# Optimization experiments

Hardware: AMD Instinct MI355X
Metric: run time of the kernel (lower is better)

Reference implementation:

```python
import jax, jax.numpy as jnp
import numpy as np

CODEBOOK_SIZE = 8192
EMBED_DIM = 128
BETA = 0.25


def setup_inputs() -> dict:
    key = jax.random.key(0)
    k1, k2 = jax.random.split(key)
    z = jax.random.normal(k1, (8, 4096, EMBED_DIM), dtype=jnp.float32)
    # nn.Embedding weight init: uniform(-1/embedding_dim, 1/embedding_dim)
    emb = jax.random.uniform(
        k2, (CODEBOOK_SIZE, EMBED_DIM), dtype=jnp.float32,
        minval=-1.0 / EMBED_DIM, maxval=1.0 / EMBED_DIM)
    return {"z": z, "emb": emb}


def reference(z, emb):
    sg = jax.lax.stop_gradient
    zf = z.reshape(-1, EMBED_DIM)                      # [N, D]
    # squared-distance: |z|^2 + |e|^2 - 2 z.e^T  -> [N, K]
    d = (jnp.sum(zf * zf, axis=1, keepdims=True)
         + jnp.sum(emb * emb, axis=1)
         - 2.0 * jnp.einsum('nd,kd->nk', zf, emb))
    idx = jnp.argmin(d, axis=1)                        # [N]
    z_q = emb[idx].reshape(z.shape)                    # gather + reshape

    # codebook usage perplexity (bincount)
    counts = jnp.zeros(CODEBOOK_SIZE, dtype=jnp.float32).at[idx].add(1.0)
    e_mean = counts / idx.size
    perplexity = jnp.exp(-jnp.sum(e_mean * jnp.log(e_mean + 1e-8)))

    commit_loss = (BETA * jnp.mean((sg(z_q) - z) ** 2)
                   + jnp.mean((z_q - sg(z)) ** 2))
    z_q_st = z + sg(z_q - z)                           # straight-through
    return z_q_st, commit_loss, perplexity
```

## Files before the change

### kernel.cpp

```cpp
#include <hip/hip_runtime.h>
#include <float.h>
#include <math.h>

#define DIM    128
#define KCB    8192
#define BT     128
#define NC     128
#define NCHUNK (KCB / NC)

typedef __attribute__((ext_vector_type(8))) short bf16x8;
typedef __attribute__((ext_vector_type(4))) float f32x4;

__device__ unsigned g_ehi[KCB * DIM / 2];
__device__ unsigned g_elo[KCB * DIM / 2];
__device__ float    g_h[KCB];
__device__ unsigned g_counts[KCB];
__device__ double   g_loss;

__device__ __forceinline__ unsigned short f2b(float x) {
    union { float f; unsigned u; } v; v.f = x;
    unsigned r = v.u + 0x7fffu + ((v.u >> 16) & 1u);
    return (unsigned short)(r >> 16);
}
__device__ __forceinline__ float b2f(unsigned short h) {
    union { unsigned u; float f; } v; v.u = ((unsigned)h) << 16; return v.f;
}
__device__ __forceinline__ void gll16(const void* g, void* l) {
    __builtin_amdgcn_global_load_lds(
        (const __attribute__((address_space(1))) void*)g,
        (__attribute__((address_space(3))) void*)l, 16, 0, 0);
}

__global__ __launch_bounds__(256) void vq_prep(const float* __restrict__ emb)
{
    const int tid  = threadIdx.x;
    const int gid  = blockIdx.x * 256 + tid;
    if (gid < KCB) g_counts[gid] = 0u;
    if (gid == 0)  g_loss = 0.0;

    const int code = (blockIdx.x << 2) + (tid >> 6);
    const int lane = tid & 63;
    const float2 v = ((const float2*)emb)[code * 64 + lane];

    unsigned short h0 = f2b(v.x), h1 = f2b(v.y);
    unsigned short l0 = f2b(v.x - b2f(h0)), l1 = f2b(v.y - b2f(h1));
    const int widx = code * 64 + (lane ^ ((code & 7) << 2));
    g_ehi[widx] = (unsigned)h0 | ((unsigned)h1 << 16);
    g_elo[widx] = (unsigned)l0 | ((unsigned)l1 << 16);

    float s = v.x * v.x + v.y * v.y;
    #pragma unroll
    for (int o = 32; o > 0; o >>= 1) s += __shfl_down(s, o);
    if (lane == 0) g_h[code] = 0.5f * s;
}

__global__ __launch_bounds__(512, 1) void vq_main(
    const float* __restrict__ z, const float* __restrict__ emb, float* __restrict__ out)
{
    __shared__ char   smem[2 * 65536];
    __shared__ float  rv[BT * 2];
    __shared__ int    ri[BT * 2];
    __shared__ int    idx_sh[BT];
    __shared__ double wred[8];

    const int tid  = threadIdx.x;
    const int lane = tid & 63;
    const int wid  = tid >> 6;
    const int tq   = wid & 3;
    const int ch2  = wid >> 2;
    const int l15  = lane & 15;
    const int lg   = lane >> 4;
    const long t0  = (long)blockIdx.x * BT;

    bf16x8 ah[2][4], al[2][4];
    #pragma unroll
    for (int m = 0; m < 2; ++m) {
        const long trow = t0 + tq * 32 + m * 16 + l15;
        #pragma unroll
        for (int kk = 0; kk < 4; ++kk) {
            const float4* zp = (const float4*)(z + trow * DIM + kk * 32 + lg * 8);
            float4 v0 = zp[0], v1 = zp[1];
            float xs[8] = {v0.x, v0.y, v0.z, v0.w, v1.x, v1.y, v1.z, v1.w};
            #pragma unroll
            for (int j = 0; j < 8; ++j) {
                unsigned short hb = f2b(xs[j]);
                ah[m][kk][j] = (short)hb;
                al[m][kk][j] = (short)f2b(xs[j] - b2f(hb));
            }
        }
    }

    const int xr = (l15 & 7) << 4;
    int loff[4];
    #pragma unroll
    for (int kk = 0; kk < 4; ++kk) loff[kk] = l15 * 256 + ((kk * 64 + lg * 16) ^ xr);
    const int nwave = ch2 * 64 * 256;

    float bv[2][4]; int bi[2][4];
    #pragma unroll
    for (int m = 0; m < 2; ++m)
        #pragma unroll
        for (int r = 0; r < 4; ++r) { bv[m][r] = FLT_MAX; bi[m][r] = 0; }

    {
        const int o = tid * 16;
        #pragma unroll
        for (int r = 0; r < 4; ++r)
            gll16((const char*)g_ehi + r * 8192 + o, smem + r * 8192 + o);
        #pragma unroll
        for (int r = 0; r < 4; ++r)
            gll16((const char*)g_elo + r * 8192 + o, smem + 32768 + r * 8192 + o);
    }
    __syncthreads();

    for (int ch = 0; ch < NCHUNK; ++ch) {
        const int cb  = ch * NC;
        const int cur = ch & 1;
        if (ch + 1 < NCHUNK) {
            const int   o  = tid * 16;
            const long  go = (long)(ch + 1) * 32768;
            char* ldst = smem + (cur ^ 1) * 65536;
            #pragma unroll
            for (int r = 0; r < 4; ++r)
                gll16((const char*)g_ehi + go + r * 8192 + o, ldst + r * 8192 + o);
            #pragma unroll
            for (int r = 0; r < 4; ++r)
                gll16((const char*)g_elo + go + r * 8192 + o, ldst + 32768 + r * 8192 + o);
        }

        const char* bhi = smem + cur * 65536 + nwave;
        const char* blo = bhi + 32768;

        #pragma unroll
        for (int n = 0; n < 4; ++n) {
            bf16x8 bh[4], bl[4];
            #pragma unroll
            for (int kk = 0; kk < 4; ++kk) {
                bh[kk] = *(const bf16x8*)(bhi + n * 4096 + loff[kk]);
                bl[kk] = *(const bf16x8*)(blo + n * 4096 + loff[kk]);
            }
            f32x4 acc[2];
            #pragma unroll
            for (int m = 0; m < 2; ++m) {
                f32x4 a = {0.f, 0.f, 0.f, 0.f};
                #pragma unroll
                for (int kk = 0; kk < 4; ++kk) {
                    a = __builtin_amdgcn_mfma_f32_16x16x32_bf16(ah[m][kk], bh[kk], a, 0, 0, 0);
                    a = __builtin_amdgcn_mfma_f32_16x16x32_bf16(al[m][kk], bh[kk], a, 0, 0, 0);
                    a = __builtin_amdgcn_mfma_f32_16x16x32_bf16(ah[m][kk], bl[kk], a, 0, 0, 0);
                }
                acc[m] = a;
            }
            const int c  = cb + ch2 * 64 + n * 16 + l15;
            const float hc = g_h[c];
            #pragma unroll
            for (int m = 0; m < 2; ++m)
                #pragma unroll
                for (int r = 0; r < 4; ++r) {
                    float sc = hc - acc[m][r];
                    if (sc < bv[m][r]) { bv[m][r] = sc; bi[m][r] = c; }
                }
        }
        __syncthreads();
    }

    #pragma unroll
    for (int m = 0; m < 2; ++m)
        #pragma unroll
        for (int r = 0; r < 4; ++r) {
            float v = bv[m][r]; int ix = bi[m][r];
            #pragma unroll
            for (int o = 1; o < 16; o <<= 1) {
                float ov = __shfl_xor(v, o);
                int   oi = __shfl_xor(ix, o);
                if (ov < v || (ov == v && oi < ix)) { v = ov; ix = oi; }
            }
            if (l15 == 0) {
                int t = tq * 32 + m * 16 + lg * 4 + r;
                rv[t * 2 + ch2] = v; ri[t * 2 + ch2] = ix;
            }
        }
    __syncthreads();
    if (tid < BT) {
        float v0 = rv[tid * 2], v1 = rv[tid * 2 + 1];
        int   i0 = ri[tid * 2], i1 = ri[tid * 2 + 1];
        int best = (v1 < v0 || (v1 == v0 && i1 < i0)) ? i1 : i0;
        idx_sh[tid] = best;
        atomicAdd(&g_counts[best], 1u);
    }
    __syncthreads();

    float lsum = 0.f;
    {
        const float4* zf4 = (const float4*)(z + t0 * DIM);
        const float4* ef4 = (const float4*)emb;
        float4*       of4 = (float4*)(out + t0 * DIM);
        #pragma unroll
        for (int r = 0; r < 8; ++r) {
            int f = r * 512 + tid;
            int t = f >> 5, dw = f & 31;
            int ci = idx_sh[t];
            float4 e4 = ef4[(size_t)ci * 32 + dw];
            float4 z4 = zf4[f];
            float dx = e4.x - z4.x, dy = e4.y - z4.y;
            float dz = e4.z - z4.z, dw2 = e4.w - z4.w;
            lsum += dx * dx + dy * dy + dz * dz + dw2 * dw2;
            float4 o;
            o.x = z4.x + dx; o.y = z4.y + dy; o.z = z4.z + dz; o.w = z4.w + dw2;
            of4[f] = o;
        }
    }
    #pragma unroll
    for (int o = 32; o > 0; o >>= 1) lsum += __shfl_down(lsum, o);
    if (lane == 0) wred[wid] = (double)lsum;
    __syncthreads();
    if (tid == 0) {
        double s = 0.0;
        #pragma unroll
        for (int w = 0; w < 8; ++w) s += wred[w];
        atomicAdd(&g_loss, s);
    }
}

__global__ __launch_bounds__(256) void vq_final(float* __restrict__ out, int n_elems, int n_tok)
{
    __shared__ double sh[4];
    const int tid = threadIdx.x;
    double s = 0.0;
    for (int i = tid; i < KCB; i += 256) {
        float em = (float)g_counts[i] / (float)n_tok;
        s += (double)(em * logf(em + 1e-8f));
    }
    #pragma unroll
    for (int o = 32; o > 0; o >>= 1) s += __shfl_down(s, o);
    if ((tid & 63) == 0) sh[tid >> 6] = s;
    __syncthreads();
    if (tid == 0) {
        double tot = sh[0] + sh[1] + sh[2] + sh[3];
        out[(size_t)n_elems]     = (float)(1.25 * g_loss / (double)n_elems);
        out[(size_t)n_elems + 1] = expf((float)(-tot));
    }
}

extern "C" void kernel_launch(void* const* d_in, const int* in_sizes, int n_in,
                              void* d_out, int out_size, void* d_ws, size_t ws_size,
                              hipStream_t stream)
{
    const float* z   = (const float*)d_in[0];
    const float* emb = (const float*)d_in[1];
    float* out = (float*)d_out;

    const int n_elems = in_sizes[0];
    const int ntok    = n_elems / DIM;

    vq_prep <<<dim3(KCB / 4),   256, 0, stream>>>(emb);
    vq_main <<<dim3(ntok / BT), 512, 0, stream>>>(z, emb, out);
    vq_final<<<dim3(1),         256, 0, stream>>>(out, n_elems, ntok);
}
```

Before: 263.5 us.

## Retile VQ distance waves to 64 tokens by 32 codes and fuse final reduction

Each wave now covers 64 tokens (4 M-tiles) against 32 codes per chunk instead of 32 tokens against 64 codes. Every B fragment loaded from LDS therefore feeds four A tiles, halving LDS reads per MFMA, and the MFMAs are interleaved across independent accumulators to hide latency. The separate final kernel is replaced by a last-block-done pattern (global atomic counter plus threadfence) inside the main kernel, saving one launch. The costs are more registers (A fragments doubled, launch bound now asks for 2 blocks per CU) and a 4-way cross-wave argmin merge instead of a 2-way one.

```diff
diff --git a/kernel.cpp b/kernel.cpp
--- a/kernel.cpp
+++ b/kernel.cpp
@@ -16,6 +16,7 @@
 __device__ float    g_h[KCB];
 __device__ unsigned g_counts[KCB];
 __device__ double   g_loss;
+__device__ unsigned g_done;
 
 __device__ __forceinline__ unsigned short f2b(float x) {
     union { float f; unsigned u; } v; v.f = x;
@@ -36,7 +37,7 @@
     const int tid  = threadIdx.x;
     const int gid  = blockIdx.x * 256 + tid;
     if (gid < KCB) g_counts[gid] = 0u;
-    if (gid == 0)  g_loss = 0.0;
+    if (gid == 0)  { g_loss = 0.0; g_done = 0u; }
 
     const int code = (blockIdx.x << 2) + (tid >> 6);
     const int lane = tid & 63;
@@ -54,28 +55,29 @@
     if (lane == 0) g_h[code] = 0.5f * s;
 }
 
-__global__ __launch_bounds__(512, 1) void vq_main(
+__global__ __launch_bounds__(512, 2) void vq_main(
     const float* __restrict__ z, const float* __restrict__ emb, float* __restrict__ out)
 {
     __shared__ char   smem[2 * 65536];
-    __shared__ float  rv[BT * 2];
-    __shared__ int    ri[BT * 2];
+    __shared__ float  rv[BT * 4];
+    __shared__ int    ri[BT * 4];
     __shared__ int    idx_sh[BT];
     __shared__ double wred[8];
+    __shared__ int    done_sh;
 
     const int tid  = threadIdx.x;
     const int lane = tid & 63;
     const int wid  = tid >> 6;
-    const int tq   = wid & 3;
-    const int ch2  = wid >> 2;
+    const int tg   = wid >> 2;
+    const int cq   = wid & 3;
     const int l15  = lane & 15;
     const int lg   = lane >> 4;
     const long t0  = (long)blockIdx.x * BT;
 
-    bf16x8 ah[2][4], al[2][4];
-    #pragma unroll
-    for (int m = 0; m < 2; ++m) {
-        const long trow = t0 + tq * 32 + m * 16 + l15;
+    bf16x8 ah[4][4], al[4][4];
+    #pragma unroll
+    for (int m = 0; m < 4; ++m) {
+        const long trow = t0 + tg * 64 + m * 16 + l15;
         #pragma unroll
         for (int kk = 0; kk < 4; ++kk) {
             const float4* zp = (const float4*)(z + trow * DIM + kk * 32 + lg * 8);
@@ -94,11 +96,10 @@
     int loff[4];
     #pragma unroll
     for (int kk = 0; kk < 4; ++kk) loff[kk] = l15 * 256 + ((kk * 64 + lg * 16) ^ xr);
-    const int nwave = ch2 * 64 * 256;
-
-    float bv[2][4]; int bi[2][4];
-    #pragma unroll
-    for (int m = 0; m < 2; ++m)
+
+    float bv[4][4]; int bi[4][4];
+    #pragma unroll
+    for (int m = 0; m < 4; ++m)
         #pragma unroll
         for (int r = 0; r < 4; ++r) { bv[m][r] = FLT_MAX; bi[m][r] = 0; }
 
@@ -117,8 +118,8 @@
         const int cb  = ch * NC;
         const int cur = ch & 1;
         if (ch + 1 < NCHUNK) {
-            const int   o  = tid * 16;
-            const long  go = (long)(ch + 1) * 32768;
+            const int  o  = tid * 16;
+            const long go = (long)(ch + 1) * 32768;
             char* ldst = smem + (cur ^ 1) * 65536;
             #pragma unroll
             for (int r = 0; r < 4; ++r)
@@ -128,36 +129,39 @@
                 gll16((const char*)g_elo + go + r * 8192 + o, ldst + 32768 + r * 8192 + o);
         }
 
-        const char* bhi = smem + cur * 65536 + nwave;
-        const char* blo = bhi + 32768;
-
-        #pragma unroll
-        for (int n = 0; n < 4; ++n) {
+        const char* base = smem + cur * 65536 + cq * 8192;
+        const int   c0   = cb + cq * 32 + l15;
+        float hc[2] = { g_h[c0], g_h[c0 + 16] };
+
+        #pragma unroll
+        for (int n = 0; n < 2; ++n) {
             bf16x8 bh[4], bl[4];
             #pragma unroll
             for (int kk = 0; kk < 4; ++kk) {
-                bh[kk] = *(const bf16x8*)(bhi + n * 4096 + loff[kk]);
-                bl[kk] = *(const bf16x8*)(blo + n * 4096 + loff[kk]);
-            }
-            f32x4 acc[2];
-            #pragma unroll
-            for (int m = 0; m < 2; ++m) {
-                f32x4 a = {0.f, 0.f, 0.f, 0.f};
-                #pragma unroll
-                for (int kk = 0; kk < 4; ++kk) {
-                    a = __builtin_amdgcn_mfma_f32_16x16x32_bf16(ah[m][kk], bh[kk], a, 0, 0, 0);
-                    a = __builtin_amdgcn_mfma_f32_16x16x32_bf16(al[m][kk], bh[kk], a, 0, 0, 0);
-                    a = __builtin_amdgcn_mfma_f32_16x16x32_bf16(ah[m][kk], bl[kk], a, 0, 0, 0);
-                }
-                acc[m] = a;
-            }
-            const int c  = cb + ch2 * 64 + n * 16 + l15;
-            const float hc = g_h[c];
-            #pragma unroll
-            for (int m = 0; m < 2; ++m)
+                bh[kk] = *(const bf16x8*)(base + n * 4096 + loff[kk]);
+                bl[kk] = *(const bf16x8*)(base + 32768 + n * 4096 + loff[kk]);
+            }
+            f32x4 acc[4];
+            #pragma unroll
+            for (int m = 0; m < 4; ++m) acc[m] = (f32x4){0.f, 0.f, 0.f, 0.f};
+            #pragma unroll
+            for (int kk = 0; kk < 4; ++kk) {
+                #pragma unroll
+                for (int m = 0; m < 4; ++m)
+                    acc[m] = __builtin_amdgcn_mfma_f32_16x16x32_bf16(ah[m][kk], bh[kk], acc[m], 0, 0, 0);
+                #pragma unroll
+                for (int m = 0; m < 4; ++m)
+                    acc[m] = __builtin_amdgcn_mfma_f32_16x16x32_bf16(al[m][kk], bh[kk], acc[m], 0, 0, 0);
+                #pragma unroll
+                for (int m = 0; m < 4; ++m)
+                    acc[m] = __builtin_amdgcn_mfma_f32_16x16x32_bf16(ah[m][kk], bl[kk], acc[m], 0, 0, 0);
+            }
+            const int c = c0 + n * 16;
+            #pragma unroll
+            for (int m = 0; m < 4; ++m)
                 #pragma unroll
                 for (int r = 0; r < 4; ++r) {
-                    float sc = hc - acc[m][r];
+                    float sc = hc[n] - acc[m][r];
                     if (sc < bv[m][r]) { bv[m][r] = sc; bi[m][r] = c; }
                 }
         }
@@ -165,7 +169,7 @@
     }
 
     #pragma unroll
-    for (int m = 0; m < 2; ++m)
+    for (int m = 0; m < 4; ++m)
         #pragma unroll
         for (int r = 0; r < 4; ++r) {
             float v = bv[m][r]; int ix = bi[m][r];
@@ -176,17 +180,20 @@
                 if (ov < v || (ov == v && oi < ix)) { v = ov; ix = oi; }
             }
             if (l15 == 0) {
-                int t = tq * 32 + m * 16 + lg * 4 + r;
-                rv[t * 2 + ch2] = v; ri[t * 2 + ch2] = ix;
+                int t = tg * 64 + m * 16 + lg * 4 + r;
+                rv[t * 4 + cq] = v; ri[t * 4 + cq] = ix;
             }
         }
     __syncthreads();
     if (tid < BT) {
-        float v0 = rv[tid * 2], v1 = rv[tid * 2 + 1];
-        int   i0 = ri[tid * 2], i1 = ri[tid * 2 + 1];
-        int best = (v1 < v0 || (v1 == v0 && i1 < i0)) ? i1 : i0;
-        idx_sh[tid] = best;
-        atomicAdd(&g_counts[best], 1u);
+        float best = rv[tid * 4]; int bidx = ri[tid * 4];
+        #pragma unroll
+        for (int x = 1; x < 4; ++x) {
+            float v = rv[tid * 4 + x]; int i = ri[tid * 4 + x];
+            if (v < best || (v == best && i < bidx)) { best = v; bidx = i; }
+        }
+        idx_sh[tid] = bidx;
+        atomicAdd(&g_counts[bidx], 1u);
     }
     __syncthreads();
 
@@ -220,25 +227,31 @@
         for (int w = 0; w < 8; ++w) s += wred[w];
         atomicAdd(&g_loss, s);
     }
-}
-
-__global__ __launch_bounds__(256) void vq_final(float* __restrict__ out, int n_elems, int n_tok)
-{
-    __shared__ double sh[4];
-    const int tid = threadIdx.x;
-    double s = 0.0;
-    for (int i = tid; i < KCB; i += 256) {
-        float em = (float)g_counts[i] / (float)n_tok;
-        s += (double)(em * logf(em + 1e-8f));
-    }
-    #pragma unroll
-    for (int o = 32; o > 0; o >>= 1) s += __shfl_down(s, o);
-    if ((tid & 63) == 0) sh[tid >> 6] = s;
-    __syncthreads();
-    if (tid == 0) {
-        double tot = sh[0] + sh[1] + sh[2] + sh[3];
-        out[(size_t)n_elems]     = (float)(1.25 * g_loss / (double)n_elems);
-        out[(size_t)n_elems + 1] = expf((float)(-tot));
+
+    __threadfence();
+    if (tid == 0) done_sh = (atomicAdd(&g_done, 1u) == gridDim.x - 1) ? 1 : 0;
+    __syncthreads();
+    if (done_sh) {
+        const int ntok    = (int)gridDim.x * BT;
+        const int n_elems = ntok * DIM;
+        double s = 0.0;
+        for (int i = tid; i < KCB; i += 512) {
+            unsigned cnt = atomicAdd(&g_counts[i], 0u);
+            float em = (float)cnt / (float)ntok;
+            s += (double)(em * logf(em + 1e-8f));
+        }
+        #pragma unroll
+        for (int o = 32; o > 0; o >>= 1) s += __shfl_down(s, o);
+        if (lane == 0) wred[wid] = s;
+        __syncthreads();
+        if (tid == 0) {
+            double tot = 0.0;
+            #pragma unroll
+            for (int w = 0; w < 8; ++w) tot += wred[w];
+            double L = atomicAdd(&g_loss, 0.0);
+            out[(size_t)n_elems]     = (float)(1.25 * L / (double)n_elems);
+            out[(size_t)n_elems + 1] = expf((float)(-tot));
+        }
     }
 }
 
@@ -253,7 +266,6 @@
     const int n_elems = in_sizes[0];
     const int ntok    = n_elems / DIM;
 
-    vq_prep <<<dim3(KCB / 4),   256, 0, stream>>>(emb);
-    vq_main <<<dim3(ntok / BT), 512, 0, stream>>>(z, emb, out);
-    vq_final<<<dim3(1),         256, 0, stream>>>(out, n_elems, ntok);
-}
+    vq_prep<<<dim3(KCB / 4),   256, 0, stream>>>(emb);
+    vq_main<<<dim3(ntok / BT), 512, 0, stream>>>(z, emb, out);
+}
```

Result: slower. 304.8 us (+15.7%).
